# Kernel tuning notes

Hardware: AMD Instinct MI355X
Metric: run time of the kernel (lower is better)

## Reference

```python
import jax, jax.numpy as jnp
import numpy as np

N_BLADES = 8
D_BLADE = 128
D_FFN = 512
LN_EPS = 1e-5


def _build_cayley_signs():
    """Cl(3,0) Cayley table: blades indexed by bitmask over {e1,e2,e3}.
    signs[i, j, k] = s where blade_i * blade_j = s * blade_k (Euclidean metric)."""
    def reorder_sign(a, b):
        a >>= 1
        total = 0
        while a:
            total += bin(a & b).count('1')
            a >>= 1
        return 1.0 if total % 2 == 0 else -1.0
    signs = np.zeros((8, 8, 8), dtype=np.float32)
    for i in range(8):
        for j in range(8):
            signs[i, j, i ^ j] = reorder_sign(i, j)
    return jnp.asarray(signs)


def setup_inputs() -> dict:
    key = jax.random.key(0)
    k_x, k_g, k_u, k_d = jax.random.split(key, 4)
    B, T = 4, 4096
    x = jax.random.normal(k_x, (B, T, N_BLADES, D_BLADE), dtype=jnp.float32)
    return {
        'x': x,
        'interaction_weights': jnp.full((N_BLADES, N_BLADES), 0.1, dtype=jnp.float32),
        'geo_gate': jnp.asarray(0.5, dtype=jnp.float32),
        'ln_w': jnp.ones((D_BLADE,), dtype=jnp.float32),
        'ln_b': jnp.zeros((D_BLADE,), dtype=jnp.float32),
        'w_gate': jax.random.normal(k_g, (D_FFN, D_BLADE), dtype=jnp.float32) * 0.02,
        'w_up': jax.random.normal(k_u, (D_FFN, D_BLADE), dtype=jnp.float32) * 0.02,
        'w_down': jax.random.normal(k_d, (D_BLADE, D_FFN), dtype=jnp.float32) * 0.02,
        'cayley_signs': _build_cayley_signs(),
    }


def reference(x, interaction_weights, geo_gate, ln_w, ln_b, w_gate, w_up, w_down, cayley_signs):
    # --- full geometric self-product via Cayley table ---
    w = jax.nn.sigmoid(interaction_weights)              # (i, j)
    signed = cayley_signs * w[:, :, None]                # (i, j, k): fold weights into sign tensor
    # result[b,t,k,d] = sum_ij signed[i,j,k] * x[b,t,i,d] * x[b,t,j,d]
    geo = jnp.einsum('btid,btjd,ijk->btkd', x, x, signed)
    # --- residual gate between geometric product and input ---
    gate = jax.nn.sigmoid(geo_gate)
    mixed = gate * geo + (1.0 - gate) * x                # (B, T, N, D)
    # --- per-blade LayerNorm over d_blade ---
    mu = jnp.mean(mixed, axis=-1, keepdims=True)
    var = jnp.mean(jnp.square(mixed - mu), axis=-1, keepdims=True)
    normed = (mixed - mu) * jax.lax.rsqrt(var + LN_EPS) * ln_w + ln_b
    # --- SwiGLU FFN (no biases) ---
    g = jnp.einsum('btnd,fd->btnf', normed, w_gate)
    u = jnp.einsum('btnd,fd->btnf', normed, w_up)
    h = jax.nn.silu(g) * u
    out = jnp.einsum('btnf,df->btnd', h, w_down)
    return x + out
```

## Files before the change

kernel.cpp:

```cpp
#include <hip/hip_runtime.h>
#include <hip/hip_bf16.h>

typedef unsigned short ushort_t;
typedef __bf16 bf16_t;
typedef bf16_t bf16x8 __attribute__((ext_vector_type(8)));
typedef unsigned short u16x8v __attribute__((ext_vector_type(8)));
typedef float f32x4 __attribute__((ext_vector_type(4)));
typedef unsigned uint32x2 __attribute__((ext_vector_type(2)));
typedef unsigned uint32x4 __attribute__((ext_vector_type(4)));

#define D 128
#define NB 8
#define DFFN 512
#define LN_EPS 1e-5f

__device__ __forceinline__ ushort_t bf16_rne(float f) {
  union { float f; unsigned u; } c; c.f = f;
  unsigned u = c.u;
  unsigned r = (u + 0x7FFFu + ((u >> 16) & 1u)) >> 16;
  return (ushort_t)r;
}

__device__ __forceinline__ unsigned cvt_pk_bf16(float lo, float hi) {
  unsigned r;
  asm("v_cvt_pk_bf16_f32 %0, %1, %2" : "=v"(r) : "v"(lo), "v"(hi));
  return r;
}

__device__ __forceinline__ bf16x8 loadfrag_bf(const ushort_t* p) {
  u16x8v v = *(const u16x8v*)p;
  return __builtin_bit_cast(bf16x8, v);
}

__device__ __forceinline__ bf16x8 load8_cvt(const float* p) {
  f32x4 a = *(const f32x4*)p;
  f32x4 b = *(const f32x4*)(p + 4);
  u16x8v r;
  r[0] = bf16_rne(a[0]); r[1] = bf16_rne(a[1]);
  r[2] = bf16_rne(a[2]); r[3] = bf16_rne(a[3]);
  r[4] = bf16_rne(b[0]); r[5] = bf16_rne(b[1]);
  r[6] = bf16_rne(b[2]); r[7] = bf16_rne(b[3]);
  return __builtin_bit_cast(bf16x8, r);
}

__device__ __forceinline__ f32x4 mfma16(bf16x8 a, bf16x8 b, f32x4 c) {
  return __builtin_amdgcn_mfma_f32_16x16x32_bf16(a, b, c, 0, 0, 0);
}

__device__ __forceinline__ float readlane_f(float v, int lane) {
  return __builtin_bit_cast(float, __builtin_amdgcn_readlane(__builtin_bit_cast(int, v), lane));
}

typedef const __attribute__((address_space(1))) void gv_t;
typedef __attribute__((address_space(3))) void lv_t;
__device__ __forceinline__ void gload_lds16(const void* g, void* l) {
  __builtin_amdgcn_global_load_lds((gv_t*)g, (lv_t*)l, 16, 0, 0);
}

__global__ void cvt_weights(const float* __restrict__ wg,
                            const float* __restrict__ wu,
                            const float* __restrict__ wd,
                            ushort_t* __restrict__ o) {
  int i = blockIdx.x * 256 + threadIdx.x;
  const int n1 = DFFN * D;
  float v;
  if (i < n1)            v = wg[i];
  else if (i < 2 * n1)   v = wu[i - n1];
  else                   v = wd[i - 2 * n1];
  o[i] = bf16_rne(v);
}

__global__ __launch_bounds__(256)
void geo_ln(const float* __restrict__ x,
            const float* __restrict__ iw,
            const float* __restrict__ geo_gate,
            const float* __restrict__ ln_w,
            const float* __restrict__ ln_b,
            const float* __restrict__ cayley,
            ushort_t* __restrict__ Aout) {
  const int tid = threadIdx.x;
  const int w = tid >> 6;
  const int l = tid & 63;
  const int g = l >> 4;
  const int q = l & 15;

  float sgv;
  {
    int i_l = l >> 3, j_l = l & 7;
    float s = cayley[(i_l * 8 + j_l) * 8 + (i_l ^ j_l)];
    sgv = s / (1.0f + __expf(-iw[i_l * 8 + j_l]));
  }
  float cd[8], cp[28];
#pragma unroll
  for (int i = 0; i < 8; ++i) cd[i] = readlane_f(sgv, i * 8 + i);
  {
    int p = 0;
#pragma unroll
    for (int i = 0; i < 8; ++i)
#pragma unroll
      for (int j = i + 1; j < 8; ++j) { cp[p] = readlane_f(sgv, i * 8 + j) + readlane_f(sgv, j * 8 + i); ++p; }
  }
  const float gate = 1.0f / (1.0f + __expf(-geo_gate[0]));
  const float ogate = 1.0f - gate;

  const f32x4 lw0 = *(const f32x4*)(ln_w + q * 8);
  const f32x4 lw1 = *(const f32x4*)(ln_w + q * 8 + 4);
  const f32x4 lb0 = *(const f32x4*)(ln_b + q * 8);
  const f32x4 lb1 = *(const f32x4*)(ln_b + q * 8 + 4);

  const long tok = (long)blockIdx.x * 16 + w * 4 + g;
  const float* xp = x + tok * (NB * D) + q * 8;

  f32x4 xa[8], xb[8];
#pragma unroll
  for (int i = 0; i < 8; ++i) { xa[i] = *(const f32x4*)(xp + i * D); xb[i] = *(const f32x4*)(xp + i * D + 4); }

  f32x4 ga[8], gb[8];
#pragma unroll
  for (int k = 0; k < 8; ++k) { ga[k] = 0.f; gb[k] = 0.f; }
#pragma unroll
  for (int i = 0; i < 8; ++i) {
    ga[0] += cd[i] * (xa[i] * xa[i]);
    gb[0] += cd[i] * (xb[i] * xb[i]);
  }
  {
    int p = 0;
#pragma unroll
    for (int i = 0; i < 8; ++i)
#pragma unroll
      for (int j = i + 1; j < 8; ++j) {
        int k = i ^ j;
        ga[k] += cp[p] * (xa[i] * xa[j]);
        gb[k] += cp[p] * (xb[i] * xb[j]);
        ++p;
      }
  }

  ushort_t* Arow0 = Aout + tok * (8 * D);
#pragma unroll
  for (int k = 0; k < 8; ++k) {
    f32x4 m0 = gate * ga[k] + ogate * xa[k];
    f32x4 m1 = gate * gb[k] + ogate * xb[k];
    float s1 = (m0[0] + m0[1]) + (m0[2] + m0[3]) + (m1[0] + m1[1]) + (m1[2] + m1[3]);
    float s2 = m0[0]*m0[0] + m0[1]*m0[1] + m0[2]*m0[2] + m0[3]*m0[3]
             + m1[0]*m1[0] + m1[1]*m1[1] + m1[2]*m1[2] + m1[3]*m1[3];
#pragma unroll
    for (int off = 8; off; off >>= 1) {
      s1 += __shfl_xor(s1, off, 64);
      s2 += __shfl_xor(s2, off, 64);
    }
    float mu = s1 * (1.0f / 128.0f);
    float rs = rsqrtf(s2 * (1.0f / 128.0f) - mu * mu + LN_EPS);
    float nb2 = -mu * rs;
    f32x4 n0, n1;
#pragma unroll
    for (int e = 0; e < 4; ++e) {
      n0[e] = (m0[e] * rs + nb2) * lw0[e] + lb0[e];
      n1[e] = (m1[e] * rs + nb2) * lw1[e] + lb1[e];
    }
    uint32x4 pk;
    pk[0] = cvt_pk_bf16(n0[0], n0[1]);
    pk[1] = cvt_pk_bf16(n0[2], n0[3]);
    pk[2] = cvt_pk_bf16(n1[0], n1[1]);
    pk[3] = cvt_pk_bf16(n1[2], n1[3]);
    *(uint32x4*)(Arow0 + k * D + ((q ^ k) * 8)) = pk;
  }
}

__global__ __launch_bounds__(256, 3)
void ffn_mfma(const ushort_t* __restrict__ Abf,
              const float* __restrict__ x,
              const ushort_t* __restrict__ wg_bf,
              const ushort_t* __restrict__ wu_bf,
              const ushort_t* __restrict__ wd_bf,
              float* __restrict__ out) {
  __shared__ ushort_t A[64 * 128];
  __shared__ ushort_t Hbuf[2][64 * 64];

  const int tid = threadIdx.x;
  const int w = tid >> 6;
  const int l = tid & 63;
  const int lg = l >> 4;
  const int ln16 = l & 15;

  const long row0 = (long)blockIdx.x * 64;

  {
    const ushort_t* src = Abf + row0 * D;
#pragma unroll
    for (int i = 0; i < 4; ++i) {
      int seg = w * 4 + i;
      gload_lds16(src + seg * 512 + l * 8, &A[seg * 512]);
    }
  }

  bf16x8 bg[4], bu[4], bd[2][2];
  {
    const int frow = w * 16 + ln16;
#pragma unroll
    for (int ks = 0; ks < 4; ++ks) {
      bg[ks] = loadfrag_bf(wg_bf + frow * D + ks * 32 + lg * 8);
      bu[ks] = loadfrag_bf(wu_bf + frow * D + ks * 32 + lg * 8);
    }
#pragma unroll
    for (int nt = 0; nt < 2; ++nt) {
      int dcol = w * 32 + nt * 16 + ln16;
#pragma unroll
      for (int k2 = 0; k2 < 2; ++k2)
        bd[nt][k2] = loadfrag_bf(wd_bf + dcol * DFFN + k2 * 32 + lg * 8);
    }
  }

  __syncthreads();

  f32x4 oacc[4][2];
#pragma unroll
  for (int mt = 0; mt < 4; ++mt)
#pragma unroll
    for (int nt = 0; nt < 2; ++nt)
#pragma unroll
      for (int r = 0; r < 4; ++r) oacc[mt][nt][r] = 0.f;

#pragma unroll
  for (int ch = 0; ch < 8; ++ch) {
    ushort_t* Hc = &Hbuf[ch & 1][0];

#pragma unroll
    for (int mt = 0; mt < 4; ++mt) {
      const int row = mt * 16 + ln16;
      f32x4 gacc = 0.f, uacc = 0.f;
#pragma unroll
      for (int ks = 0; ks < 4; ++ks) {
        int unit = (ks * 4 + lg) ^ (row & 7);
        bf16x8 a = *(const bf16x8*)&A[row * 128 + unit * 8];
        gacc = mfma16(bg[ks], a, gacc);
        uacc = mfma16(bu[ks], a, uacc);
      }
      float h0 = gacc[0] / (1.0f + __expf(-gacc[0])) * uacc[0];
      float h1 = gacc[1] / (1.0f + __expf(-gacc[1])) * uacc[1];
      float h2 = gacc[2] / (1.0f + __expf(-gacc[2])) * uacc[2];
      float h3 = gacc[3] / (1.0f + __expf(-gacc[3])) * uacc[3];
      uint32x2 pk;
      pk[0] = cvt_pk_bf16(h0, h1);
      pk[1] = cvt_pk_bf16(h2, h3);
      const int m = row;
      int u = (w * 2 + (lg >> 1)) ^ (m & 7);
      *(uint32x2*)((char*)Hc + m * 128 + u * 16 + (lg & 1) * 8) = pk;
    }

    __syncthreads();

    bf16x8 nbg[4], nbu[4];
    if (ch < 7) {
      const int frow = (ch + 1) * 64 + w * 16 + ln16;
#pragma unroll
      for (int ks = 0; ks < 4; ++ks) {
        nbg[ks] = loadfrag_bf(wg_bf + frow * D + ks * 32 + lg * 8);
        nbu[ks] = loadfrag_bf(wu_bf + frow * D + ks * 32 + lg * 8);
      }
    }

#pragma unroll
    for (int mt = 0; mt < 4; ++mt) {
      const int m = mt * 16 + ln16;
#pragma unroll
      for (int k2 = 0; k2 < 2; ++k2) {
        int u = (k2 * 4 + lg) ^ (m & 7);
        bf16x8 hf = *(const bf16x8*)((const char*)Hc + m * 128 + u * 16);
        oacc[mt][0] = mfma16(hf, bd[0][k2], oacc[mt][0]);
        oacc[mt][1] = mfma16(hf, bd[1][k2], oacc[mt][1]);
      }
    }

    if (ch < 7) {
#pragma unroll
      for (int nt = 0; nt < 2; ++nt) {
        int dcol = w * 32 + nt * 16 + ln16;
#pragma unroll
        for (int k2 = 0; k2 < 2; ++k2)
          bd[nt][k2] = loadfrag_bf(wd_bf + dcol * DFFN + (ch + 1) * 64 + k2 * 32 + lg * 8);
      }
#pragma unroll
      for (int ks = 0; ks < 4; ++ks) { bg[ks] = nbg[ks]; bu[ks] = nbu[ks]; }
    }
  }

#pragma unroll
  for (int mt = 0; mt < 4; ++mt) {
#pragma unroll
    for (int r = 0; r < 4; ++r) {
      long rowg = row0 + mt * 16 + lg * 4 + r;
      const float* xp = x + rowg * D;
      float* op = out + rowg * D;
#pragma unroll
      for (int nt = 0; nt < 2; ++nt) {
        int d = w * 32 + nt * 16 + ln16;
        op[d] = xp[d] + oacc[mt][nt][r];
      }
    }
  }
}

template <bool WS_BF16>
__global__ __launch_bounds__(256, 2)
void fused_geo_ffn(const float* __restrict__ x,
                   const float* __restrict__ iw,
                   const float* __restrict__ geo_gate,
                   const float* __restrict__ ln_w,
                   const float* __restrict__ ln_b,
                   const float* __restrict__ w_gate_f,
                   const float* __restrict__ w_up_f,
                   const float* __restrict__ w_down_f,
                   const float* __restrict__ cayley,
                   const ushort_t* __restrict__ wg_bf,
                   const ushort_t* __restrict__ wu_bf,
                   const ushort_t* __restrict__ wd_bf,
                   float* __restrict__ out) {
  __shared__ float sg[64];
  __shared__ ushort_t A_lds[128 * 128];
  __shared__ ushort_t H_lds[128 * 64];

  const int tid = threadIdx.x;
  const int w = tid >> 6;
  const int l = tid & 63;
  const int lg = l >> 4;
  const int ln16 = l & 15;
  const int kbase = lg * 8;

  if (tid < 64) {
    int i = tid >> 3, j = tid & 7;
    float s = cayley[(i * 8 + j) * 8 + (i ^ j)];
    sg[tid] = s / (1.0f + __expf(-iw[i * 8 + j]));
  }
  __syncthreads();
  float sgr[64];
#pragma unroll
  for (int t = 0; t < 64; ++t) sgr[t] = sg[t];

  const float gate = 1.0f / (1.0f + __expf(-geo_gate[0]));
  const float2 lw = *(const float2*)(ln_w + 2 * l);
  const float2 lb = *(const float2*)(ln_b + 2 * l);
  const long tok0 = (long)blockIdx.x * 16;

  for (int tt = 0; tt < 4; ++tt) {
    int ltok = w * 4 + tt;
    const float* xp = x + (tok0 + ltok) * (long)(NB * D);
    float2 xv[8];
#pragma unroll
    for (int i = 0; i < 8; ++i) xv[i] = *(const float2*)(xp + i * D + 2 * l);
#pragma unroll
    for (int k = 0; k < 8; ++k) {
      float2 g; g.x = 0.f; g.y = 0.f;
#pragma unroll
      for (int i = 0; i < 8; ++i) {
        float s = sgr[i * 8 + (i ^ k)];
        g.x += s * xv[i].x * xv[i ^ k].x;
        g.y += s * xv[i].y * xv[i ^ k].y;
      }
      float2 m;
      m.x = gate * g.x + (1.0f - gate) * xv[k].x;
      m.y = gate * g.y + (1.0f - gate) * xv[k].y;
      float s1 = m.x + m.y;
      float s2 = m.x * m.x + m.y * m.y;
#pragma unroll
      for (int off = 32; off; off >>= 1) {
        s1 += __shfl_xor(s1, off, 64);
        s2 += __shfl_xor(s2, off, 64);
      }
      float mu = s1 * (1.0f / 128.0f);
      float rs = rsqrtf(s2 * (1.0f / 128.0f) - mu * mu + LN_EPS);
      float nx = (m.x - mu) * rs * lw.x + lb.x;
      float ny = (m.y - mu) * rs * lw.y + lb.y;
      int row = ltok * 8 + k;
      int colb = (4 * l) ^ ((row & 7) << 4);
      *(unsigned*)((char*)A_lds + row * 256 + colb) = cvt_pk_bf16(nx, ny);
    }
  }
  __syncthreads();

  f32x4 oacc[8][2];
#pragma unroll
  for (int mt = 0; mt < 8; ++mt)
#pragma unroll
    for (int nt = 0; nt < 2; ++nt)
#pragma unroll
      for (int r = 0; r < 4; ++r) oacc[mt][nt][r] = 0.f;

  for (int ch = 0; ch < 8; ++ch) {
    const int fbase = ch * 64 + w * 16 + ln16;
    bf16x8 bg[4], bu[4];
#pragma unroll
    for (int ks = 0; ks < 4; ++ks) {
      int koff = ks * 32 + kbase;
      if (WS_BF16) {
        bg[ks] = loadfrag_bf(wg_bf + fbase * D + koff);
        bu[ks] = loadfrag_bf(wu_bf + fbase * D + koff);
      } else {
        bg[ks] = load8_cvt(w_gate_f + fbase * D + koff);
        bu[ks] = load8_cvt(w_up_f + fbase * D + koff);
      }
    }
#pragma unroll
    for (int mt = 0; mt < 8; ++mt) {
      const int row = mt * 16 + ln16;
      f32x4 gacc = 0.f, uacc = 0.f;
#pragma unroll
      for (int ks = 0; ks < 4; ++ks) {
        int colb = ((ks * 32 + kbase) * 2) ^ ((row & 7) << 4);
        bf16x8 a = *(const bf16x8*)((const char*)A_lds + row * 256 + colb);
        gacc = mfma16(bg[ks], a, gacc);
        uacc = mfma16(bu[ks], a, uacc);
      }
      float h[4];
#pragma unroll
      for (int r = 0; r < 4; ++r) {
        float gv = gacc[r], uv = uacc[r];
        h[r] = gv / (1.0f + __expf(-gv)) * uv;
      }
      uint32x2 pk;
      pk[0] = cvt_pk_bf16(h[0], h[1]);
      pk[1] = cvt_pk_bf16(h[2], h[3]);
      int u = (w * 2 + (lg >> 1)) ^ (row & 7);
      *(uint32x2*)&H_lds[row * 64 + u * 8 + (lg & 1) * 4] = pk;
    }
    __syncthreads();
#pragma unroll
    for (int mt = 0; mt < 8; ++mt) {
      const int row = mt * 16 + ln16;
#pragma unroll
      for (int ks = 0; ks < 2; ++ks) {
        int u = (ks * 4 + lg) ^ (row & 7);
        bf16x8 hfrag = *(const bf16x8*)&H_lds[row * 64 + u * 8];
        bf16x8 b0, b1;
        int dcol0 = w * 32 + ln16;
        int foff = ch * 64 + ks * 32 + kbase;
        if (WS_BF16) {
          b0 = loadfrag_bf(wd_bf + dcol0 * DFFN + foff);
          b1 = loadfrag_bf(wd_bf + (dcol0 + 16) * DFFN + foff);
        } else {
          b0 = load8_cvt(w_down_f + dcol0 * DFFN + foff);
          b1 = load8_cvt(w_down_f + (dcol0 + 16) * DFFN + foff);
        }
        oacc[mt][0] = mfma16(hfrag, b0, oacc[mt][0]);
        oacc[mt][1] = mfma16(hfrag, b1, oacc[mt][1]);
      }
    }
    __syncthreads();
  }

  const long rowg0 = tok0 * NB;
#pragma unroll
  for (int mt = 0; mt < 8; ++mt) {
#pragma unroll
    for (int r = 0; r < 4; ++r) {
      long row = rowg0 + mt * 16 + lg * 4 + r;
      const float* xp = x + row * D;
      float* op = out + row * D;
#pragma unroll
      for (int nt = 0; nt < 2; ++nt) {
        int d = w * 32 + nt * 16 + ln16;
        op[d] = xp[d] + oacc[mt][nt][r];
      }
    }
  }
}

extern "C" void kernel_launch(void* const* d_in, const int* in_sizes, int n_in,
                              void* d_out, int out_size, void* d_ws, size_t ws_size,
                              hipStream_t stream) {
  const float* x   = (const float*)d_in[0];
  const float* iw  = (const float*)d_in[1];
  const float* gg  = (const float*)d_in[2];
  const float* lnw = (const float*)d_in[3];
  const float* lnb = (const float*)d_in[4];
  const float* wg  = (const float*)d_in[5];
  const float* wu  = (const float*)d_in[6];
  const float* wd  = (const float*)d_in[7];
  const float* cs  = (const float*)d_in[8];
  float* out = (float*)d_out;

  const int ntok = in_sizes[0] / (NB * D);
  const int wtot = 3 * DFFN * D;
  const size_t wbytes = (size_t)wtot * 2;
  const size_t abytes = (size_t)ntok * NB * D * 2;

  if (ws_size >= wbytes + abytes) {
    ushort_t* wbf = (ushort_t*)d_ws;
    ushort_t* act = wbf + wtot;
    cvt_weights<<<wtot / 256, 256, 0, stream>>>(wg, wu, wd, wbf);
    geo_ln<<<ntok / 16, 256, 0, stream>>>(x, iw, gg, lnw, lnb, cs, act);
    ffn_mfma<<<(ntok * NB) / 64, 256, 0, stream>>>(
        act, x, wbf, wbf + DFFN * D, wbf + 2 * DFFN * D, out);
  } else if (ws_size >= wbytes) {
    ushort_t* wbf = (ushort_t*)d_ws;
    cvt_weights<<<wtot / 256, 256, 0, stream>>>(wg, wu, wd, wbf);
    fused_geo_ffn<true><<<ntok / 16, 256, 0, stream>>>(
        x, iw, gg, lnw, lnb, wg, wu, wd, cs,
        wbf, wbf + DFFN * D, wbf + 2 * DFFN * D, out);
  } else {
    fused_geo_ffn<false><<<ntok / 16, 256, 0, stream>>>(
        x, iw, gg, lnw, lnb, wg, wu, wd, cs,
        (const ushort_t*)nullptr, (const ushort_t*)nullptr, (const ushort_t*)nullptr, out);
  }
}
```

Before: 134.5 us.

## Hoist A fragments to registers, alias LDS for H, use fast reciprocal in SiLU

The FFN kernel now loads all A-tile MFMA fragments from LDS into registers once, then reuses that 16KB LDS region as the double-buffered H scratch. This cuts LDS per block from 32KB to 16KB, which could allow more resident blocks, and removes repeated A reads from LDS in every chunk. Next-chunk gate/up weight loads are issued straight into the live registers once the MFMAs finish, and SiLU uses the hardware rcp instead of a full divide. In exchange it holds 16 extra bf16x8 fragments per thread, which raises register pressure and may reduce occupancy or cause spills. The rcp also slightly changes numerics.

```diff
diff --git a/kernel.cpp b/kernel.cpp
--- a/kernel.cpp
+++ b/kernel.cpp
@@ -49,6 +49,10 @@
 
 __device__ __forceinline__ float readlane_f(float v, int lane) {
   return __builtin_bit_cast(float, __builtin_amdgcn_readlane(__builtin_bit_cast(int, v), lane));
+}
+
+__device__ __forceinline__ float fast_rcp(float x) {
+  return __builtin_amdgcn_rcpf(x);
 }
 
 typedef const __attribute__((address_space(1))) void gv_t;
@@ -174,8 +178,7 @@
               const ushort_t* __restrict__ wu_bf,
               const ushort_t* __restrict__ wd_bf,
               float* __restrict__ out) {
-  __shared__ ushort_t A[64 * 128];
-  __shared__ ushort_t Hbuf[2][64 * 64];
+  __shared__ ushort_t SMEM[64 * 128];
 
   const int tid = threadIdx.x;
   const int w = tid >> 6;
@@ -190,7 +193,7 @@
 #pragma unroll
     for (int i = 0; i < 4; ++i) {
       int seg = w * 4 + i;
-      gload_lds16(src + seg * 512 + l * 8, &A[seg * 512]);
+      gload_lds16(src + seg * 512 + l * 8, &SMEM[seg * 512]);
     }
   }
 
@@ -213,6 +216,19 @@
 
   __syncthreads();
 
+  bf16x8 afr[4][4];
+#pragma unroll
+  for (int mt = 0; mt < 4; ++mt) {
+    const int row = mt * 16 + ln16;
+#pragma unroll
+    for (int ks = 0; ks < 4; ++ks) {
+      int unit = (ks * 4 + lg) ^ (row & 7);
+      afr[mt][ks] = *(const bf16x8*)&SMEM[row * 128 + unit * 8];
+    }
+  }
+
+  __syncthreads();
+
   f32x4 oacc[4][2];
 #pragma unroll
   for (int mt = 0; mt < 4; ++mt)
@@ -223,42 +239,46 @@
 
 #pragma unroll
   for (int ch = 0; ch < 8; ++ch) {
-    ushort_t* Hc = &Hbuf[ch & 1][0];
-
+    ushort_t* Hc = SMEM + (ch & 1) * 4096;
+
+    f32x4 gacc[4], uacc[4];
 #pragma unroll
     for (int mt = 0; mt < 4; ++mt) {
-      const int row = mt * 16 + ln16;
-      f32x4 gacc = 0.f, uacc = 0.f;
+      gacc[mt] = 0.f; uacc[mt] = 0.f;
 #pragma unroll
       for (int ks = 0; ks < 4; ++ks) {
-        int unit = (ks * 4 + lg) ^ (row & 7);
-        bf16x8 a = *(const bf16x8*)&A[row * 128 + unit * 8];
-        gacc = mfma16(bg[ks], a, gacc);
-        uacc = mfma16(bu[ks], a, uacc);
-      }
-      float h0 = gacc[0] / (1.0f + __expf(-gacc[0])) * uacc[0];
-      float h1 = gacc[1] / (1.0f + __expf(-gacc[1])) * uacc[1];
-      float h2 = gacc[2] / (1.0f + __expf(-gacc[2])) * uacc[2];
-      float h3 = gacc[3] / (1.0f + __expf(-gacc[3])) * uacc[3];
+        gacc[mt] = mfma16(bg[ks], afr[mt][ks], gacc[mt]);
+        uacc[mt] = mfma16(bu[ks], afr[mt][ks], uacc[mt]);
+      }
+    }
+
+    if (ch < 7) {
+      const int frow = (ch + 1) * 64 + w * 16 + ln16;
+#pragma unroll
+      for (int ks = 0; ks < 4; ++ks) {
+        bg[ks] = loadfrag_bf(wg_bf + frow * D + ks * 32 + lg * 8);
+        bu[ks] = loadfrag_bf(wu_bf + frow * D + ks * 32 + lg * 8);
+      }
+    }
+
+#pragma unroll
+    for (int mt = 0; mt < 4; ++mt) {
+      const int m = mt * 16 + ln16;
+      float h[4];
+#pragma unroll
+      for (int r = 0; r < 4; ++r) {
+        float gv = gacc[mt][r];
+        float s = fast_rcp(1.0f + __expf(-gv));
+        h[r] = gv * s * uacc[mt][r];
+      }
       uint32x2 pk;
-      pk[0] = cvt_pk_bf16(h0, h1);
-      pk[1] = cvt_pk_bf16(h2, h3);
-      const int m = row;
+      pk[0] = cvt_pk_bf16(h[0], h[1]);
+      pk[1] = cvt_pk_bf16(h[2], h[3]);
       int u = (w * 2 + (lg >> 1)) ^ (m & 7);
       *(uint32x2*)((char*)Hc + m * 128 + u * 16 + (lg & 1) * 8) = pk;
     }
 
     __syncthreads();
-
-    bf16x8 nbg[4], nbu[4];
-    if (ch < 7) {
-      const int frow = (ch + 1) * 64 + w * 16 + ln16;
-#pragma unroll
-      for (int ks = 0; ks < 4; ++ks) {
-        nbg[ks] = loadfrag_bf(wg_bf + frow * D + ks * 32 + lg * 8);
-        nbu[ks] = loadfrag_bf(wu_bf + frow * D + ks * 32 + lg * 8);
-      }
-    }
 
 #pragma unroll
     for (int mt = 0; mt < 4; ++mt) {
@@ -280,8 +300,6 @@
         for (int k2 = 0; k2 < 2; ++k2)
           bd[nt][k2] = loadfrag_bf(wd_bf + dcol * DFFN + (ch + 1) * 64 + k2 * 32 + lg * 8);
       }
-#pragma unroll
-      for (int ks = 0; ks < 4; ++ks) { bg[ks] = nbg[ks]; bu[ks] = nbu[ks]; }
     }
   }
 
@@ -415,7 +433,7 @@
 #pragma unroll
       for (int r = 0; r < 4; ++r) {
         float gv = gacc[r], uv = uacc[r];
-        h[r] = gv / (1.0f + __expf(-gv)) * uv;
+        h[r] = gv * __builtin_amdgcn_rcpf(1.0f + __expf(-gv)) * uv;
       }
       uint32x2 pk;
       pk[0] = cvt_pk_bf16(h[0], h[1]);
```

Result: faster. 125.2 us (-6.9%).
